# Kernel tuning notes

Hardware: AMD Instinct MI355X
Metric: run time of the kernel (lower is better)

The kernel has to match this reference:

```python
import jax, jax.numpy as jnp
import numpy as np

NEIGHBOR_NUM = 32  # init kwarg neighbor_num

B, N, C = 64, 512, 1024

def setup_inputs() -> dict:
    key = jax.random.key(0)
    x = jax.random.normal(key, (B, N, C), dtype=jnp.float32)
    return {"x": x}

def reference(x):
    # si = x @ x^T (detached in the original -> stop_gradient)
    si = jax.lax.stop_gradient(x)
    si = jnp.einsum('bic,bjc->bij', si, si)  # (b, n, n)
    # k-th largest value per row as threshold
    topv, _ = jax.lax.top_k(si, NEIGHBOR_NUM)          # (b, n, k)
    threshold = topv[..., -1:]                          # (b, n, 1)
    adj = (si >= threshold).astype(si.dtype)            # (b, n, n)
    # normalize_digraph: D^{-1/2} A D^{-1/2} with D = row-degree diag
    node_degrees = adj.sum(axis=-1)                     # (b, n)
    degs_inv_sqrt = node_degrees ** (-0.5)              # (b, n)
    # diag(d) @ A @ diag(d) == d_i * A_ij * d_j
    norm_A = degs_inv_sqrt[:, :, None] * adj * degs_inv_sqrt[:, None, :]
    return norm_A
```

## Files before the change

kernel.cpp:

```cpp
#include <hip/hip_runtime.h>
#include <hip/hip_bf16.h>
#include <math.h>

#define B 64
#define N 512
#define C 1024
#define K_NEIGH 32
#define DELTA 0.9f
#define BISECT_ITERS 12

typedef __attribute__((ext_vector_type(8))) _Float16 half8;
typedef __attribute__((ext_vector_type(4))) float f32x4;

__device__ __forceinline__ half8 cvt8(float4 a, float4 b) {
    half8 g;
    g[0] = (_Float16)a.x; g[1] = (_Float16)a.y; g[2] = (_Float16)a.z; g[3] = (_Float16)a.w;
    g[4] = (_Float16)b.x; g[5] = (_Float16)b.y; g[6] = (_Float16)b.z; g[7] = (_Float16)b.w;
    return g;
}

__global__ __launch_bounds__(512, 2) void gemm_f16(const float* __restrict__ x,
                                                   _Float16* __restrict__ S16) {
    __shared__ half8 Ah[2][1024];
    __shared__ half8 Bh[2][1024];

    const int id   = blockIdx.x;
    const int xcd  = id & 7;
    const int slot = id >> 3;
    const int b    = xcd * 8 + (slot >> 2);
    const int tile = slot & 3;
    const int ti = tile >> 1, tj = tile & 1;
    const int row0 = ti * 256;
    const int col0 = tj * 256;
    const float* xb = x + (size_t)b * N * C;
    const bool diag = (ti == tj);

    const int t    = threadIdx.x;
    const int w    = t >> 6;
    const int lane = t & 63;
    const int quad = lane >> 4;
    const int lid  = lane & 15;
    const int wr   = (w >> 2) * 128;
    const int wc   = (w & 3) * 64;

    const int srow = t >> 1;
    const int s0   = (t & 1) * 2;
    const int koff = (t & 1) * 16;

    f32x4 acc[8][4];
#pragma unroll
    for (int r = 0; r < 8; r++)
#pragma unroll
        for (int c = 0; c < 4; c++)
#pragma unroll
            for (int e = 0; e < 4; e++) acc[r][c][e] = 0.f;

    const float* pArow = xb + (size_t)(row0 + srow) * C + koff;
    const float* pBrow = xb + (size_t)(col0 + srow) * C + koff;

    float4 ra[4], rb[4];
    {
        const float4* pa = (const float4*)pArow;
#pragma unroll
        for (int i = 0; i < 4; i++) ra[i] = pa[i];
        if (!diag) {
            const float4* pb = (const float4*)pBrow;
#pragma unroll
            for (int i = 0; i < 4; i++) rb[i] = pb[i];
        }
        Ah[0][s0 * 256 + srow]       = cvt8(ra[0], ra[1]);
        Ah[0][(s0 + 1) * 256 + srow] = cvt8(ra[2], ra[3]);
        if (!diag) {
            Bh[0][s0 * 256 + srow]       = cvt8(rb[0], rb[1]);
            Bh[0][(s0 + 1) * 256 + srow] = cvt8(rb[2], rb[3]);
        }
    }
    __syncthreads();

    int cur = 0;
    const int NIT = C / 32;
    for (int it = 0; it < NIT; ++it) {
        const bool more = (it + 1) < NIT;
        if (more) {
            const float4* pa = (const float4*)(pArow + (it + 1) * 32);
#pragma unroll
            for (int i = 0; i < 4; i++) ra[i] = pa[i];
            if (!diag) {
                const float4* pb = (const float4*)(pBrow + (it + 1) * 32);
#pragma unroll
                for (int i = 0; i < 4; i++) rb[i] = pb[i];
            }
        }
        const half8* Ab = &Ah[cur][0];
        const half8* Bb = diag ? Ab : &Bh[cur][0];
        half8 vb[4];
#pragma unroll
        for (int c = 0; c < 4; c++) vb[c] = Bb[quad * 256 + wc + c * 16 + lid];
        __builtin_amdgcn_s_setprio(1);
#pragma unroll
        for (int r = 0; r < 8; r++) {
            half8 va = Ab[quad * 256 + wr + r * 16 + lid];
#pragma unroll
            for (int c = 0; c < 4; c++)
                acc[r][c] = __builtin_amdgcn_mfma_f32_16x16x32_f16(va, vb[c], acc[r][c], 0, 0, 0);
        }
        __builtin_amdgcn_s_setprio(0);
        if (more) {
            const int nb = cur ^ 1;
            Ah[nb][s0 * 256 + srow]       = cvt8(ra[0], ra[1]);
            Ah[nb][(s0 + 1) * 256 + srow] = cvt8(ra[2], ra[3]);
            if (!diag) {
                Bh[nb][s0 * 256 + srow]       = cvt8(rb[0], rb[1]);
                Bh[nb][(s0 + 1) * 256 + srow] = cvt8(rb[2], rb[3]);
            }
        }
        __syncthreads();
        cur ^= 1;
    }

    _Float16* Sb = S16 + (size_t)b * N * N;
#pragma unroll
    for (int r = 0; r < 8; r++) {
#pragma unroll
        for (int c = 0; c < 4; c++) {
#pragma unroll
            for (int e = 0; e < 4; e++) {
                const int grow = row0 + wr + r * 16 + quad * 4 + e;
                const int gcol = col0 + wc + c * 16 + lid;
                Sb[(size_t)grow * N + gcol] = (_Float16)acc[r][c][e];
            }
        }
    }
}

__global__ __launch_bounds__(256) void thresh_mask(const _Float16* __restrict__ S16,
                                                   const float* __restrict__ x,
                                                   unsigned long long* __restrict__ masks,
                                                   float* __restrict__ dinv) {
    const int id   = blockIdx.x;
    const int xcd  = id & 7;
    const int slot = id >> 3;
    const int bsw  = xcd * 8 + (slot >> 7);
    const int rblk = slot & 127;
    const int row  = bsw * N + rblk * 4 + (threadIdx.x >> 6);
    const int lane = threadIdx.x & 63;
    const _Float16* Srow = S16 + (size_t)row * N;

    float v0[8];
#pragma unroll
    for (int k = 0; k < 8; k++) v0[k] = (float)Srow[lane + 64 * k];

    float lo = -1400.f, hi = 1400.f;
    for (int it = 0; it < BISECT_ITERS; it++) {
        const float mid = 0.5f * (lo + hi);
        int c = 0;
#pragma unroll
        for (int k = 0; k < 8; k++) c += __popcll(__ballot(v0[k] > mid));
        if (c >= K_NEIGH) lo = mid; else hi = mid;
    }
    const float P   = 0.5f * (lo + hi);
    const float hiB = P + DELTA, loB = P - DELTA;

    int cA = 0;
#pragma unroll
    for (int k = 0; k < 8; k++) cA += __popcll(__ballot(v0[k] > hiB));
    const int m_need = K_NEIGH - cA;

    int cnt = 0, myj = -1;
#pragma unroll
    for (int kq = 0; kq < 8; kq++) {
        unsigned long long bm = __ballot(v0[kq] >= loB && v0[kq] <= hiB);
        while (bm) {
            int bl = __ffsll(bm) - 1;
            bm &= bm - 1;
            if (cnt == lane) myj = bl + 64 * kq;
            cnt++;
        }
    }
    const int nc = cnt < 64 ? cnt : 64;

    const int bb_ = row >> 9, ii = row & (N - 1);
    const float* xi = x + ((size_t)bb_ * N + ii) * C;
    float4 ai[4];
#pragma unroll
    for (int q = 0; q < 4; q++) ai[q] = *(const float4*)(xi + q * 256 + lane * 4);

    float ex = -INFINITY;
    for (int c2 = 0; c2 < nc; c2++) {
        const int j = __shfl(myj, c2);
        const float* xj = x + ((size_t)bb_ * N + j) * C;
        float s = 0.f;
#pragma unroll
        for (int q = 0; q < 4; q++) {
            float4 bv = *(const float4*)(xj + q * 256 + lane * 4);
            s = fmaf(ai[q].x, bv.x, s);
            s = fmaf(ai[q].y, bv.y, s);
            s = fmaf(ai[q].z, bv.z, s);
            s = fmaf(ai[q].w, bv.w, s);
        }
#pragma unroll
        for (int off = 32; off > 0; off >>= 1) s += __shfl_xor(s, off);
        if (lane == c2) ex = s;
    }

    float val = ex, T = -INFINITY;
    for (int it = 0; it < m_need; it++) {
        float M = val;
#pragma unroll
        for (int off = 32; off > 0; off >>= 1) M = fmaxf(M, __shfl_xor(M, off));
        T = M;
        unsigned long long ball = __ballot(val == M);
        int first = __ffsll(ball) - 1;
        if (lane == first) val = -INFINITY;
    }
    const int dec = (lane < nc && ex >= T) ? 1 : 0;

    int bits[8];
#pragma unroll
    for (int kq = 0; kq < 8; kq++) bits[kq] = (v0[kq] > hiB) ? 1 : 0;
    for (int c2 = 0; c2 < nc; c2++) {
        int j = __shfl(myj, c2);
        int d = __shfl(dec, c2);
        if ((j & 63) == lane) bits[j >> 6] = d;
    }

    unsigned long long msk[8];
    int deg = 0;
#pragma unroll
    for (int kq = 0; kq < 8; kq++) {
        msk[kq] = __ballot(bits[kq] != 0);
        deg += __popcll(msk[kq]);
    }
    if (lane == 0) {
#pragma unroll
        for (int kq = 0; kq < 8; kq++) masks[(size_t)row * 8 + kq] = msk[kq];
        dinv[row] = rsqrtf((float)deg);
    }
}

__global__ __launch_bounds__(256) void scale_adj(float* __restrict__ Sout,
                                                 const unsigned long long* __restrict__ masks,
                                                 const float* __restrict__ dinv) {
    const int idx = blockIdx.x * 256 + threadIdx.x;
    const int jq = idx & 127;
    const int i  = (idx >> 7) & (N - 1);
    const int b  = idx >> 16;
    const int row = (b << 9) | i;
    const int j0 = jq * 4;

    const unsigned long long mk = masks[(size_t)row * 8 + (j0 >> 6)];
    const float di = dinv[row];
    float4 dj = ((const float4*)dinv)[(b << 7) | jq];

    float4 o;
    o.x = ((mk >> ((j0 + 0) & 63)) & 1ull) ? di * dj.x : 0.f;
    o.y = ((mk >> ((j0 + 1) & 63)) & 1ull) ? di * dj.y : 0.f;
    o.z = ((mk >> ((j0 + 2) & 63)) & 1ull) ? di * dj.z : 0.f;
    o.w = ((mk >> ((j0 + 3) & 63)) & 1ull) ? di * dj.w : 0.f;
    ((float4*)Sout)[idx] = o;
}

extern "C" void kernel_launch(void* const* d_in, const int* in_sizes, int n_in,
                              void* d_out, int out_size, void* d_ws, size_t ws_size,
                              hipStream_t stream) {
    const float* x = (const float*)d_in[0];
    float* out = (float*)d_out;
    _Float16* S16 = (_Float16*)d_out;
    unsigned long long* masks = (unsigned long long*)d_ws;
    float* dinv = (float*)(masks + (size_t)B * N * 8);

    gemm_f16<<<dim3(B * 4), 512, 0, stream>>>(x, S16);
    thresh_mask<<<B * N / 4, 256, 0, stream>>>(S16, x, masks, dinv);
    const int total4 = B * N * N / 4;
    scale_adj<<<total4 / 256, 256, 0, stream>>>(out, masks, dinv);
}
```

Baseline: 272.5 us.

## Double GEMM block to 1024 threads with smaller per-wave tiles and two-stage register prefetch

The GEMM block grows from 512 to 1024 threads (16 waves), and each wave now computes a 64x64 sub-tile instead of 128x64, which halves the accumulator registers per thread. Each thread loads and converts half as much global data per K-step. The main loop is unrolled by two, with two register prefetch sets issued two steps ahead to hide global latency. The aim is more waves in flight to hide memory and LDS latency, at the cost of more LDS read traffic per MFMA and more barrier synchronization across a larger block.

```diff
diff --git a/kernel.cpp b/kernel.cpp
--- a/kernel.cpp
+++ b/kernel.cpp
@@ -19,8 +19,26 @@
     return g;
 }
 
-__global__ __launch_bounds__(512, 2) void gemm_f16(const float* __restrict__ x,
-                                                   _Float16* __restrict__ S16) {
+__device__ __forceinline__ void mfma_step(const half8* __restrict__ Ab,
+                                          const half8* __restrict__ Bb,
+                                          f32x4 (&acc)[4][4],
+                                          int quad, int lid, int wr, int wc) {
+    half8 vb[4];
+#pragma unroll
+    for (int c = 0; c < 4; c++) vb[c] = Bb[quad * 256 + wc + c * 16 + lid];
+    __builtin_amdgcn_s_setprio(1);
+#pragma unroll
+    for (int r = 0; r < 4; r++) {
+        half8 va = Ab[quad * 256 + wr + r * 16 + lid];
+#pragma unroll
+        for (int c = 0; c < 4; c++)
+            acc[r][c] = __builtin_amdgcn_mfma_f32_16x16x32_f16(va, vb[c], acc[r][c], 0, 0, 0);
+    }
+    __builtin_amdgcn_s_setprio(0);
+}
+
+__global__ __launch_bounds__(1024, 4) void gemm_f16(const float* __restrict__ x,
+                                                    _Float16* __restrict__ S16) {
     __shared__ half8 Ah[2][1024];
     __shared__ half8 Bh[2][1024];
 
@@ -40,16 +58,17 @@
     const int lane = t & 63;
     const int quad = lane >> 4;
     const int lid  = lane & 15;
-    const int wr   = (w >> 2) * 128;
+    const int wr   = (w >> 2) * 64;
     const int wc   = (w & 3) * 64;
 
-    const int srow = t >> 1;
-    const int s0   = (t & 1) * 2;
-    const int koff = (t & 1) * 16;
-
-    f32x4 acc[8][4];
-#pragma unroll
-    for (int r = 0; r < 8; r++)
+    const int srow = t >> 2;
+    const int sg   = t & 3;
+    const int gidx = sg * 256 + srow;
+    const int koff = sg * 8;
+
+    f32x4 acc[4][4];
+#pragma unroll
+    for (int r = 0; r < 4; r++)
 #pragma unroll
         for (int c = 0; c < 4; c++)
 #pragma unroll
@@ -58,69 +77,50 @@
     const float* pArow = xb + (size_t)(row0 + srow) * C + koff;
     const float* pBrow = xb + (size_t)(col0 + srow) * C + koff;
 
-    float4 ra[4], rb[4];
-    {
-        const float4* pa = (const float4*)pArow;
-#pragma unroll
-        for (int i = 0; i < 4; i++) ra[i] = pa[i];
-        if (!diag) {
-            const float4* pb = (const float4*)pBrow;
-#pragma unroll
-            for (int i = 0; i < 4; i++) rb[i] = pb[i];
-        }
-        Ah[0][s0 * 256 + srow]       = cvt8(ra[0], ra[1]);
-        Ah[0][(s0 + 1) * 256 + srow] = cvt8(ra[2], ra[3]);
-        if (!diag) {
-            Bh[0][s0 * 256 + srow]       = cvt8(rb[0], rb[1]);
-            Bh[0][(s0 + 1) * 256 + srow] = cvt8(rb[2], rb[3]);
-        }
-    }
+#define LOADX(A0, A1, B0, B1, step)                                          \
+    {                                                                        \
+        const float4* pa = (const float4*)(pArow + (step) * 32);             \
+        A0 = pa[0]; A1 = pa[1];                                              \
+        if (!diag) {                                                         \
+            const float4* pb = (const float4*)(pBrow + (step) * 32);         \
+            B0 = pb[0]; B1 = pb[1];                                          \
+        }                                                                    \
+    }
+#define STOREX(buf, A0, A1, B0, B1)                                          \
+    {                                                                        \
+        Ah[buf][gidx] = cvt8(A0, A1);                                        \
+        if (!diag) Bh[buf][gidx] = cvt8(B0, B1);                             \
+    }
+
+    float4 Xa0, Xa1, Xb0, Xb1, Ya0, Ya1, Yb0, Yb1;
+
+    LOADX(Xa0, Xa1, Xb0, Xb1, 0);
+    STOREX(0, Xa0, Xa1, Xb0, Xb1);
+    LOADX(Ya0, Ya1, Yb0, Yb1, 1);
     __syncthreads();
 
-    int cur = 0;
     const int NIT = C / 32;
-    for (int it = 0; it < NIT; ++it) {
-        const bool more = (it + 1) < NIT;
-        if (more) {
-            const float4* pa = (const float4*)(pArow + (it + 1) * 32);
-#pragma unroll
-            for (int i = 0; i < 4; i++) ra[i] = pa[i];
-            if (!diag) {
-                const float4* pb = (const float4*)(pBrow + (it + 1) * 32);
-#pragma unroll
-                for (int i = 0; i < 4; i++) rb[i] = pb[i];
-            }
-        }
-        const half8* Ab = &Ah[cur][0];
-        const half8* Bb = diag ? Ab : &Bh[cur][0];
-        half8 vb[4];
-#pragma unroll
-        for (int c = 0; c < 4; c++) vb[c] = Bb[quad * 256 + wc + c * 16 + lid];
-        __builtin_amdgcn_s_setprio(1);
-#pragma unroll
-        for (int r = 0; r < 8; r++) {
-            half8 va = Ab[quad * 256 + wr + r * 16 + lid];
-#pragma unroll
-            for (int c = 0; c < 4; c++)
-                acc[r][c] = __builtin_amdgcn_mfma_f32_16x16x32_f16(va, vb[c], acc[r][c], 0, 0, 0);
-        }
-        __builtin_amdgcn_s_setprio(0);
-        if (more) {
-            const int nb = cur ^ 1;
-            Ah[nb][s0 * 256 + srow]       = cvt8(ra[0], ra[1]);
-            Ah[nb][(s0 + 1) * 256 + srow] = cvt8(ra[2], ra[3]);
-            if (!diag) {
-                Bh[nb][s0 * 256 + srow]       = cvt8(rb[0], rb[1]);
-                Bh[nb][(s0 + 1) * 256 + srow] = cvt8(rb[2], rb[3]);
-            }
-        }
+    for (int it = 0; it < NIT - 2; it += 2) {
+        LOADX(Xa0, Xa1, Xb0, Xb1, it + 2);
+        mfma_step(&Ah[0][0], diag ? &Ah[0][0] : &Bh[0][0], acc, quad, lid, wr, wc);
+        STOREX(1, Ya0, Ya1, Yb0, Yb1);
         __syncthreads();
-        cur ^= 1;
-    }
+        LOADX(Ya0, Ya1, Yb0, Yb1, it + 3);
+        mfma_step(&Ah[1][0], diag ? &Ah[1][0] : &Bh[1][0], acc, quad, lid, wr, wc);
+        STOREX(0, Xa0, Xa1, Xb0, Xb1);
+        __syncthreads();
+    }
+    mfma_step(&Ah[0][0], diag ? &Ah[0][0] : &Bh[0][0], acc, quad, lid, wr, wc);
+    STOREX(1, Ya0, Ya1, Yb0, Yb1);
+    __syncthreads();
+    mfma_step(&Ah[1][0], diag ? &Ah[1][0] : &Bh[1][0], acc, quad, lid, wr, wc);
+
+#undef LOADX
+#undef STOREX
 
     _Float16* Sb = S16 + (size_t)b * N * N;
 #pragma unroll
-    for (int r = 0; r < 8; r++) {
+    for (int r = 0; r < 4; r++) {
 #pragma unroll
         for (int c = 0; c < 4; c++) {
 #pragma unroll
@@ -269,7 +269,7 @@
     unsigned long long* masks = (unsigned long long*)d_ws;
     float* dinv = (float*)(masks + (size_t)B * N * 8);
 
-    gemm_f16<<<dim3(B * 4), 512, 0, stream>>>(x, S16);
+    gemm_f16<<<dim3(B * 4), 1024, 0, stream>>>(x, S16);
     thresh_mask<<<B * N / 4, 256, 0, stream>>>(S16, x, masks, dinv);
     const int total4 = B * N * N / 4;
     scale_adj<<<total4 / 256, 256, 0, stream>>>(out, masks, dinv);
```

After: 310.5 us. +13.9%, slower.
